# Kernel optimization log

Hardware: AMD Instinct MI355X
Metric: run time of the kernel (lower is better)

The kernel has to match this reference:

```python
import jax, jax.numpy as jnp
import numpy as np

B = 8192
T = 1000
STATE_DIM = 3
HIDDEN = 256
DT = 0.01


def setup_inputs() -> dict:
    key = jax.random.key(0)
    ks = jax.random.split(key, 7)
    initial_state = jax.random.normal(ks[0], (B, STATE_DIM), dtype=jnp.float32)
    t_grid = (jnp.arange(T, dtype=jnp.float32) * DT)
    s = 0.1  # small init scale keeps the ODE well-behaved over the grid
    W1 = jax.random.normal(ks[1], (STATE_DIM, HIDDEN), dtype=jnp.float32) * s
    b1 = jnp.zeros((HIDDEN,), dtype=jnp.float32)
    W2 = jax.random.normal(ks[2], (HIDDEN, HIDDEN), dtype=jnp.float32) * s
    b2 = jnp.zeros((HIDDEN,), dtype=jnp.float32)
    W3 = jax.random.normal(ks[3], (HIDDEN, STATE_DIM), dtype=jnp.float32) * s
    b3 = jnp.zeros((STATE_DIM,), dtype=jnp.float32)
    return {"initial_state": initial_state, "t_grid": t_grid,
            "W1": W1, "b1": b1, "W2": W2, "b2": b2, "W3": W3, "b3": b3}


def reference(initial_state, t_grid, W1, b1, W2, b2, W3, b3):
    # VectorFieldNet: state -> tanh MLP -> dstate/dt (autonomous; ignores t)
    def vf(s):  # s: [B, D]
        h = jnp.tanh(s @ W1 + b1)
        h = jnp.tanh(h @ W2 + b2)
        return h @ W3 + b3

    dts = t_grid[1:] - t_grid[:-1]  # [T-1]

    def step(cur, dt):
        k1 = vf(cur)
        k2 = vf(cur + 0.5 * dt * k1)
        k3 = vf(cur + 0.5 * dt * k2)
        k4 = vf(cur + dt * k3)
        nxt = cur + (dt / 6.0) * (k1 + 2.0 * k2 + 2.0 * k3 + k4)
        return nxt, nxt

    _, traj = jax.lax.scan(step, initial_state, dts)  # [T-1, B, D]
    rollout = jnp.concatenate([initial_state[None], traj], axis=0)  # [T, B, D]
    return jnp.transpose(rollout, (1, 0, 2))  # [B, T, D]
```

## Files before the change

kernel.cpp:

```cpp
#include <hip/hip_runtime.h>

typedef __attribute__((ext_vector_type(8))) short bf16x8;
typedef __attribute__((ext_vector_type(4))) float f32x4;
typedef __attribute__((ext_vector_type(2))) unsigned int uint2v;

union FU { unsigned int u[4]; uint4 q; bf16x8 v; };

__device__ inline unsigned int cvt_pk(float lo, float hi) {
    unsigned int r;
    asm("v_cvt_pk_bf16_f32 %0, %1, %2" : "=v"(r) : "v"(lo), "v"(hi));
    return r;
}

#define TWO_LOG2E 2.8853900817779268f
__device__ inline float tanh_fast(float x) {
#if __has_builtin(__builtin_amdgcn_exp2f)
    float e = __builtin_amdgcn_exp2f(x * TWO_LOG2E);
#else
    float e = __expf(x + x);
#endif
    return fmaf(-2.f, __builtin_amdgcn_rcpf(e + 1.f), 1.f);
}

__device__ inline float xor32_add(float p) {
    float c = p;
    asm("v_permlane32_swap_b32 %0, %1" : "+v"(c), "+v"(p));
    return p + c;
}

__device__ inline float xor16_add(float p) {
#if __has_builtin(__builtin_amdgcn_permlane16_swap)
    uint2v r = __builtin_amdgcn_permlane16_swap(__float_as_uint(p),
                                                __float_as_uint(p),
                                                false, false);
    return __uint_as_float(r[0]) + __uint_as_float(r[1]);
#else
    return p + __shfl_xor(p, 16);
#endif
}

__device__ inline void lds_barrier() {
    asm volatile("s_waitcnt lgkmcnt(0)\n\ts_barrier" ::: "memory");
}

#define TS 1000
#define ROWU 33
#define P2ROW 208

__global__ __launch_bounds__(512, 4)
void node_ode_kernel(const float* __restrict__ Ig, const float* __restrict__ tg,
                     const float* __restrict__ W1g, const float* __restrict__ b1g,
                     const float* __restrict__ W2g, const float* __restrict__ b2g,
                     const float* __restrict__ W3g, const float* __restrict__ b3g,
                     float* __restrict__ outp)
{
    __shared__ __align__(16) uint4 h1q[16 * ROWU];
    __shared__ __align__(16) char part2[16 * P2ROW];
    __shared__ float dtss[TS - 1];

    const int tid  = threadIdx.x;
    const int lane = tid & 63;
    const int wv   = tid >> 6;
    const int nb   = lane & 15;
    const int g4   = lane >> 4;
    const int bb0  = blockIdx.x * 16;

    const int wbase = nb * ROWU + wv * 4 + g4;
    const int rbase = nb * ROWU + g4;
    char* const prow = part2 + nb * P2ROW;

    for (int i = tid; i < TS - 1; i += 512) dtss[i] = tg[i + 1] - tg[i];

    const float b30 = b3g[0], b31 = b3g[1], b32 = b3g[2];

    float4 b2r0 = *(const float4*)&b2g[wv * 32 + g4 * 4];
    float4 b2r1 = *(const float4*)&b2g[wv * 32 + 16 + g4 * 4];

    float y00 = Ig[(bb0 + nb) * 3 + 0];
    float y01 = Ig[(bb0 + nb) * 3 + 1];
    float y02 = Ig[(bb0 + nb) * 3 + 2];
    if (tid < 16) {
        size_t o = (size_t)(bb0 + tid) * (TS * 3);
        outp[o + 0] = y00; outp[o + 1] = y01; outp[o + 2] = y02;
    }

    bf16x8 w2f[2][8];
    {
        const int ncb = wv * 32 + nb;
        #pragma unroll
        for (int mt = 0; mt < 2; ++mt) {
            #pragma unroll
            for (int ks = 0; ks < 8; ++ks) {
                FU f;
                #pragma unroll
                for (int jj = 0; jj < 4; ++jj) {
                    int k0 = ks * 32 + g4 * 8 + jj * 2;
                    f.u[jj] = cvt_pk(W2g[(size_t)k0 * 256 + ncb + mt * 16],
                                     W2g[(size_t)(k0 + 1) * 256 + ncb + mt * 16]);
                }
                w2f[mt][ks] = f.v;
            }
        }
    }

    bf16x8 w1a[2];
    {
        const int colb = wv * 32 + ((nb >> 2) << 3) + (nb & 3);
        #pragma unroll
        for (int mt = 0; mt < 2; ++mt) {
            const int col = colb + mt * 4;
            float w0 = W1g[col], w1 = W1g[256 + col], w2 = W1g[512 + col];
            float bb = b1g[col];
            FU f;
            if (g4 == 0) {
                f.u[0] = cvt_pk(w0, w1);
                f.u[1] = cvt_pk(w2, w0);
                f.u[2] = cvt_pk(w1, w2);
                f.u[3] = cvt_pk(bb, 0.f);
            } else if (g4 == 1) {
                unsigned int p01 = cvt_pk(w0, w1);
                unsigned int p2x = cvt_pk(w2, 0.f);
                float w0l = w0 - __uint_as_float(p01 << 16);
                float w1l = w1 - __uint_as_float(p01 & 0xFFFF0000u);
                float w2l = w2 - __uint_as_float(p2x << 16);
                f.u[0] = cvt_pk(w0l, w1l);
                f.u[1] = cvt_pk(w2l, 0.f);
                f.u[2] = 0u; f.u[3] = 0u;
            } else {
                f.u[0] = f.u[1] = f.u[2] = f.u[3] = 0u;
            }
            w1a[mt] = f.v;
        }
    }

    bf16x8 w3a;
    {
        FU f; f.u[0] = f.u[1] = f.u[2] = f.u[3] = 0u;
        if (nb < 6) {
            const int d = (nb < 3) ? nb : nb - 3;
            float w[8];
            #pragma unroll
            for (int j = 0; j < 8; ++j) {
                int ch = (j < 4) ? (wv * 32 + 4 * g4 + j)
                                 : (wv * 32 + 16 + 4 * g4 + (j - 4));
                w[j] = W3g[ch * 3 + d];
            }
            #pragma unroll
            for (int p = 0; p < 4; ++p) {
                unsigned int hp = cvt_pk(w[2 * p], w[2 * p + 1]);
                if (nb < 3) {
                    f.u[p] = hp;
                } else {
                    float l0 = w[2 * p]     - __uint_as_float(hp << 16);
                    float l1 = w[2 * p + 1] - __uint_as_float(hp & 0xFFFF0000u);
                    f.u[p] = cvt_pk(l0, l1);
                }
            }
        }
        w3a = f.v;
    }
    __syncthreads();

    auto EVAL = [&](float ycx, float ycy, float ycz,
                    float& kkx, float& kky, float& kkz) {
        {
            unsigned int u01  = cvt_pk(ycx, ycy);
            float yl0 = ycx - __uint_as_float(u01 << 16);
            float yl1 = ycy - __uint_as_float(u01 & 0xFFFF0000u);
            unsigned int u2l0 = cvt_pk(ycz, yl0);
            float yl2 = ycz - __uint_as_float(u2l0 << 16);
            unsigned int ull  = cvt_pk(yl1, yl2);
            FU bf;
            if (g4 == 0) {
                bf.u[0] = u01; bf.u[1] = u2l0; bf.u[2] = ull; bf.u[3] = 0x00003f80u;
            } else if (g4 == 1) {
                bf.u[0] = u01; bf.u[1] = u2l0 & 0x0000FFFFu; bf.u[2] = 0u; bf.u[3] = 0u;
            } else {
                bf.u[0] = bf.u[1] = bf.u[2] = bf.u[3] = 0u;
            }
            f32x4 dA = {0.f, 0.f, 0.f, 0.f};
            f32x4 dB = {0.f, 0.f, 0.f, 0.f};
            dA = __builtin_amdgcn_mfma_f32_16x16x32_bf16(w1a[0], bf.v, dA, 0, 0, 0);
            dB = __builtin_amdgcn_mfma_f32_16x16x32_bf16(w1a[1], bf.v, dB, 0, 0, 0);
            uint4 wq;
            wq.x = cvt_pk(tanh_fast(dA[0]), tanh_fast(dA[1]));
            wq.y = cvt_pk(tanh_fast(dA[2]), tanh_fast(dA[3]));
            wq.z = cvt_pk(tanh_fast(dB[0]), tanh_fast(dB[1]));
            wq.w = cvt_pk(tanh_fast(dB[2]), tanh_fast(dB[3]));
            h1q[wbase] = wq;
        }
        lds_barrier();

        {
            f32x4 acc0 = {b2r0.x, b2r0.y, b2r0.z, b2r0.w};
            f32x4 acc1 = {b2r1.x, b2r1.y, b2r1.z, b2r1.w};
            #pragma unroll
            for (int ks = 0; ks < 8; ++ks) {
                FU tm; tm.q = h1q[rbase + ks * 4];
                acc0 = __builtin_amdgcn_mfma_f32_16x16x32_bf16(w2f[0][ks], tm.v, acc0, 0, 0, 0);
                acc1 = __builtin_amdgcn_mfma_f32_16x16x32_bf16(w2f[1][ks], tm.v, acc1, 0, 0, 0);
            }
            FU pb;
            pb.u[0] = cvt_pk(tanh_fast(acc0[0]), tanh_fast(acc0[1]));
            pb.u[1] = cvt_pk(tanh_fast(acc0[2]), tanh_fast(acc0[3]));
            pb.u[2] = cvt_pk(tanh_fast(acc1[0]), tanh_fast(acc1[1]));
            pb.u[3] = cvt_pk(tanh_fast(acc1[2]), tanh_fast(acc1[3]));
            f32x4 pd = {0.f, 0.f, 0.f, 0.f};
            pd = __builtin_amdgcn_mfma_f32_16x16x32_bf16(w3a, pb.v, pd, 0, 0, 0);
            if (g4 == 0)
                *(float4*)(prow + wv * 16) = make_float4(pd[0], pd[1], pd[2], pd[3]);
            else if (g4 == 1)
                *(float2*)(prow + 128 + wv * 8) = make_float2(pd[0], pd[1]);
        }
        lds_barrier();

        {
            float4 q1 = *(const float4*)(prow + g4 * 16);
            float4 q2 = *(const float4*)(prow + 64 + g4 * 16);
            float4 q3 = *(const float4*)(prow + 128 + g4 * 16);
            float k0 = (q1.x + q2.x) + (q1.w + q2.w);
            float k1 = (q1.y + q2.y) + (q3.x + q3.z);
            float k2 = (q1.z + q2.z) + (q3.y + q3.w);
            k0 = xor16_add(k0); k1 = xor16_add(k1); k2 = xor16_add(k2);
            kkx = xor32_add(k0) + b30;
            kky = xor32_add(k1) + b31;
            kkz = xor32_add(k2) + b32;
        }
    };

    for (int t = 0; t < TS - 1; ++t) {
        const float dtc = dtss[t];
        const float hh = 0.5f * dtc;
        float k1x, k1y, k1z, k2x, k2y, k2z, k3x, k3y, k3z, k4x, k4y, k4z;
        EVAL(y00, y01, y02, k1x, k1y, k1z);
        EVAL(fmaf(hh, k1x, y00), fmaf(hh, k1y, y01), fmaf(hh, k1z, y02),
             k2x, k2y, k2z);
        EVAL(fmaf(hh, k2x, y00), fmaf(hh, k2y, y01), fmaf(hh, k2z, y02),
             k3x, k3y, k3z);
        EVAL(fmaf(dtc, k3x, y00), fmaf(dtc, k3y, y01), fmaf(dtc, k3z, y02),
             k4x, k4y, k4z);
        const float s = dtc * (1.f / 6.f);
        y00 = fmaf(s, (k1x + k4x) + 2.f * (k2x + k3x), y00);
        y01 = fmaf(s, (k1y + k4y) + 2.f * (k2y + k3y), y01);
        y02 = fmaf(s, (k1z + k4z) + 2.f * (k2z + k3z), y02);
        if ((wv == (t & 7)) && lane < 16) {
            size_t o = (size_t)(bb0 + nb) * (TS * 3) + (size_t)(t + 1) * 3;
            outp[o + 0] = y00; outp[o + 1] = y01; outp[o + 2] = y02;
        }
    }
}

extern "C" void kernel_launch(void* const* d_in, const int* in_sizes, int n_in,
                              void* d_out, int out_size, void* d_ws, size_t ws_size,
                              hipStream_t stream) {
    (void)in_sizes; (void)n_in; (void)d_ws; (void)ws_size; (void)out_size;
    const float* Ig  = (const float*)d_in[0];
    const float* tg  = (const float*)d_in[1];
    const float* W1g = (const float*)d_in[2];
    const float* b1g = (const float*)d_in[3];
    const float* W2g = (const float*)d_in[4];
    const float* b2g = (const float*)d_in[5];
    const float* W3g = (const float*)d_in[6];
    const float* b3g = (const float*)d_in[7];
    float* outp = (float*)d_out;

    dim3 grid(512), block(512);
    hipLaunchKernelGGL(node_ode_kernel, grid, block, 0, stream,
                       Ig, tg, W1g, b1g, W2g, b2g, W3g, b3g, outp);
}
```

Baseline: 7.271 ms.

## Interleave two batch tiles per block to overlap RK4 stage pipelines

Each block now handles 32 rows as two independent 16-row tiles, and the two tiles' MLP evaluations are software-pipelined across double-buffered LDS. The aim is to hide the serial dependency and barrier latency of each RK stage by running one tile's layer-2/3 work while the other tile's layer-1 and reduction proceed, cutting barriers per evaluation from three to two. The grid is halved to 256 blocks and launch bounds drop to 2 blocks per CU. That lowers the number of concurrent independent blocks and may raise register pressure.

```diff
diff --git a/kernel.cpp b/kernel.cpp
--- a/kernel.cpp
+++ b/kernel.cpp
@@ -44,18 +44,19 @@
 }
 
 #define TS 1000
+#define NEV ((TS - 1) * 4)
 #define ROWU 33
 #define P2ROW 208
 
-__global__ __launch_bounds__(512, 4)
+__global__ __launch_bounds__(512, 2)
 void node_ode_kernel(const float* __restrict__ Ig, const float* __restrict__ tg,
                      const float* __restrict__ W1g, const float* __restrict__ b1g,
                      const float* __restrict__ W2g, const float* __restrict__ b2g,
                      const float* __restrict__ W3g, const float* __restrict__ b3g,
                      float* __restrict__ outp)
 {
-    __shared__ __align__(16) uint4 h1q[16 * ROWU];
-    __shared__ __align__(16) char part2[16 * P2ROW];
+    __shared__ __align__(16) uint4 h1q[2][16 * ROWU];
+    __shared__ __align__(16) char part2[2][16 * P2ROW];
     __shared__ float dtss[TS - 1];
 
     const int tid  = threadIdx.x;
@@ -63,25 +64,35 @@
     const int wv   = tid >> 6;
     const int nb   = lane & 15;
     const int g4   = lane >> 4;
-    const int bb0  = blockIdx.x * 16;
-
-    const int wbase = nb * ROWU + wv * 4 + g4;
-    const int rbase = nb * ROWU + g4;
-    char* const prow = part2 + nb * P2ROW;
+    const int bb0  = blockIdx.x * 32;
+
+    const int wslot = nb * ROWU + wv * 4 + g4;
+    const int rslot = nb * ROWU + g4;
+    char* const prow0 = part2[0] + nb * P2ROW;
+    char* const prow1 = part2[1] + nb * P2ROW;
 
     for (int i = tid; i < TS - 1; i += 512) dtss[i] = tg[i + 1] - tg[i];
 
     const float b30 = b3g[0], b31 = b3g[1], b32 = b3g[2];
-
     float4 b2r0 = *(const float4*)&b2g[wv * 32 + g4 * 4];
     float4 b2r1 = *(const float4*)&b2g[wv * 32 + 16 + g4 * 4];
 
-    float y00 = Ig[(bb0 + nb) * 3 + 0];
-    float y01 = Ig[(bb0 + nb) * 3 + 1];
-    float y02 = Ig[(bb0 + nb) * 3 + 2];
-    if (tid < 16) {
+    float y0_0 = Ig[(bb0 + nb) * 3 + 0];
+    float y0_1 = Ig[(bb0 + nb) * 3 + 1];
+    float y0_2 = Ig[(bb0 + nb) * 3 + 2];
+    float y1_0 = Ig[(bb0 + 16 + nb) * 3 + 0];
+    float y1_1 = Ig[(bb0 + 16 + nb) * 3 + 1];
+    float y1_2 = Ig[(bb0 + 16 + nb) * 3 + 2];
+    float yc0_0 = y0_0, yc0_1 = y0_1, yc0_2 = y0_2;
+    float yc1_0 = y1_0, yc1_1 = y1_1, yc1_2 = y1_2;
+    float ks0_0 = 0.f, ks0_1 = 0.f, ks0_2 = 0.f;
+    float ks1_0 = 0.f, ks1_1 = 0.f, ks1_2 = 0.f;
+    if (tid < 32) {
         size_t o = (size_t)(bb0 + tid) * (TS * 3);
-        outp[o + 0] = y00; outp[o + 1] = y01; outp[o + 2] = y02;
+        float a0 = Ig[(bb0 + tid) * 3 + 0];
+        float a1 = Ig[(bb0 + tid) * 3 + 1];
+        float a2 = Ig[(bb0 + tid) * 3 + 2];
+        outp[o + 0] = a0; outp[o + 1] = a1; outp[o + 2] = a2;
     }
 
     bf16x8 w2f[2][8];
@@ -161,92 +172,126 @@
     }
     __syncthreads();
 
-    auto EVAL = [&](float ycx, float ycy, float ycz,
-                    float& kkx, float& kky, float& kkz) {
+    auto stageA = [&](float ycx, float ycy, float ycz, uint4* hb) {
+        unsigned int u01  = cvt_pk(ycx, ycy);
+        float yl0 = ycx - __uint_as_float(u01 << 16);
+        float yl1 = ycy - __uint_as_float(u01 & 0xFFFF0000u);
+        unsigned int u2l0 = cvt_pk(ycz, yl0);
+        float yl2 = ycz - __uint_as_float(u2l0 << 16);
+        unsigned int ull  = cvt_pk(yl1, yl2);
+        FU bf;
+        if (g4 == 0) {
+            bf.u[0] = u01; bf.u[1] = u2l0; bf.u[2] = ull; bf.u[3] = 0x00003f80u;
+        } else if (g4 == 1) {
+            bf.u[0] = u01; bf.u[1] = u2l0 & 0x0000FFFFu; bf.u[2] = 0u; bf.u[3] = 0u;
+        } else {
+            bf.u[0] = bf.u[1] = bf.u[2] = bf.u[3] = 0u;
+        }
+        f32x4 dA = {0.f, 0.f, 0.f, 0.f};
+        f32x4 dB = {0.f, 0.f, 0.f, 0.f};
+        dA = __builtin_amdgcn_mfma_f32_16x16x32_bf16(w1a[0], bf.v, dA, 0, 0, 0);
+        dB = __builtin_amdgcn_mfma_f32_16x16x32_bf16(w1a[1], bf.v, dB, 0, 0, 0);
+        uint4 wq;
+        wq.x = cvt_pk(tanh_fast(dA[0]), tanh_fast(dA[1]));
+        wq.y = cvt_pk(tanh_fast(dA[2]), tanh_fast(dA[3]));
+        wq.z = cvt_pk(tanh_fast(dB[0]), tanh_fast(dB[1]));
+        wq.w = cvt_pk(tanh_fast(dB[2]), tanh_fast(dB[3]));
+        hb[wslot] = wq;
+    };
+
+    auto stageB = [&](const uint4* hb, char* pw) {
+        f32x4 acc0 = {b2r0.x, b2r0.y, b2r0.z, b2r0.w};
+        f32x4 acc1 = {b2r1.x, b2r1.y, b2r1.z, b2r1.w};
+        #pragma unroll
+        for (int ks = 0; ks < 8; ++ks) {
+            FU tm; tm.q = hb[rslot + ks * 4];
+            acc0 = __builtin_amdgcn_mfma_f32_16x16x32_bf16(w2f[0][ks], tm.v, acc0, 0, 0, 0);
+            acc1 = __builtin_amdgcn_mfma_f32_16x16x32_bf16(w2f[1][ks], tm.v, acc1, 0, 0, 0);
+        }
+        FU pb;
+        pb.u[0] = cvt_pk(tanh_fast(acc0[0]), tanh_fast(acc0[1]));
+        pb.u[1] = cvt_pk(tanh_fast(acc0[2]), tanh_fast(acc0[3]));
+        pb.u[2] = cvt_pk(tanh_fast(acc1[0]), tanh_fast(acc1[1]));
+        pb.u[3] = cvt_pk(tanh_fast(acc1[2]), tanh_fast(acc1[3]));
+        f32x4 pd = {0.f, 0.f, 0.f, 0.f};
+        pd = __builtin_amdgcn_mfma_f32_16x16x32_bf16(w3a, pb.v, pd, 0, 0, 0);
+        if (g4 == 0)
+            *(float4*)(pw + wv * 16) = make_float4(pd[0], pd[1], pd[2], pd[3]);
+        else if (g4 == 1)
+            *(float2*)(pw + 128 + wv * 8) = make_float2(pd[0], pd[1]);
+    };
+
+    auto combine = [&](const char* pr, float& kkx, float& kky, float& kkz) {
+        float4 q1 = *(const float4*)(pr + g4 * 16);
+        float4 q2 = *(const float4*)(pr + 64 + g4 * 16);
+        float4 q3 = *(const float4*)(pr + 128 + g4 * 16);
+        float k0 = (q1.x + q2.x) + (q1.w + q2.w);
+        float k1 = (q1.y + q2.y) + (q3.x + q3.z);
+        float k2 = (q1.z + q2.z) + (q3.y + q3.w);
+        k0 = xor16_add(k0); k1 = xor16_add(k1); k2 = xor16_add(k2);
+        kkx = xor32_add(k0) + b30;
+        kky = xor32_add(k1) + b31;
+        kkz = xor32_add(k2) + b32;
+    };
+
+    auto advance = [&](int ev, float k0, float k1, float k2,
+                       float& y0, float& y1, float& y2,
+                       float& ks0, float& ks1, float& ks2,
+                       float& yc0, float& yc1, float& yc2, int rowoff) {
+        const int pph = ev & 3;
+        const int t = ev >> 2;
+        float dtc = dtss[t];
+        if (pph == 0) {
+            ks0 = k0; ks1 = k1; ks2 = k2;
+            float h = 0.5f * dtc;
+            yc0 = fmaf(h, k0, y0); yc1 = fmaf(h, k1, y1); yc2 = fmaf(h, k2, y2);
+        } else if (pph == 1) {
+            ks0 += 2.f * k0; ks1 += 2.f * k1; ks2 += 2.f * k2;
+            float h = 0.5f * dtc;
+            yc0 = fmaf(h, k0, y0); yc1 = fmaf(h, k1, y1); yc2 = fmaf(h, k2, y2);
+        } else if (pph == 2) {
+            ks0 += 2.f * k0; ks1 += 2.f * k1; ks2 += 2.f * k2;
+            yc0 = fmaf(dtc, k0, y0); yc1 = fmaf(dtc, k1, y1); yc2 = fmaf(dtc, k2, y2);
+        } else {
+            float s = dtc * (1.f / 6.f);
+            y0 = fmaf(s, ks0 + k0, y0);
+            y1 = fmaf(s, ks1 + k1, y1);
+            y2 = fmaf(s, ks2 + k2, y2);
+            yc0 = y0; yc1 = y1; yc2 = y2;
+            if ((wv == (t & 7)) && lane < 16) {
+                size_t o = (size_t)(bb0 + rowoff + nb) * (TS * 3) + (size_t)(t + 1) * 3;
+                outp[o + 0] = y0; outp[o + 1] = y1; outp[o + 2] = y2;
+            }
+        }
+    };
+
+    stageA(yc0_0, yc0_1, yc0_2, h1q[0]);
+    lds_barrier();
+    for (int ev = 0; ev < NEV; ++ev) {
+        stageB(h1q[0], prow0);
+        if (ev > 0) {
+            float k0, k1, k2;
+            combine(prow1, k0, k1, k2);
+            advance(ev - 1, k0, k1, k2, y1_0, y1_1, y1_2,
+                    ks1_0, ks1_1, ks1_2, yc1_0, yc1_1, yc1_2, 16);
+        }
+        stageA(yc1_0, yc1_1, yc1_2, h1q[1]);
+        lds_barrier();
+        stageB(h1q[1], prow1);
         {
-            unsigned int u01  = cvt_pk(ycx, ycy);
-            float yl0 = ycx - __uint_as_float(u01 << 16);
-            float yl1 = ycy - __uint_as_float(u01 & 0xFFFF0000u);
-            unsigned int u2l0 = cvt_pk(ycz, yl0);
-            float yl2 = ycz - __uint_as_float(u2l0 << 16);
-            unsigned int ull  = cvt_pk(yl1, yl2);
-            FU bf;
-            if (g4 == 0) {
-                bf.u[0] = u01; bf.u[1] = u2l0; bf.u[2] = ull; bf.u[3] = 0x00003f80u;
-            } else if (g4 == 1) {
-                bf.u[0] = u01; bf.u[1] = u2l0 & 0x0000FFFFu; bf.u[2] = 0u; bf.u[3] = 0u;
-            } else {
-                bf.u[0] = bf.u[1] = bf.u[2] = bf.u[3] = 0u;
-            }
-            f32x4 dA = {0.f, 0.f, 0.f, 0.f};
-            f32x4 dB = {0.f, 0.f, 0.f, 0.f};
-            dA = __builtin_amdgcn_mfma_f32_16x16x32_bf16(w1a[0], bf.v, dA, 0, 0, 0);
-            dB = __builtin_amdgcn_mfma_f32_16x16x32_bf16(w1a[1], bf.v, dB, 0, 0, 0);
-            uint4 wq;
-            wq.x = cvt_pk(tanh_fast(dA[0]), tanh_fast(dA[1]));
-            wq.y = cvt_pk(tanh_fast(dA[2]), tanh_fast(dA[3]));
-            wq.z = cvt_pk(tanh_fast(dB[0]), tanh_fast(dB[1]));
-            wq.w = cvt_pk(tanh_fast(dB[2]), tanh_fast(dB[3]));
-            h1q[wbase] = wq;
-        }
+            float k0, k1, k2;
+            combine(prow0, k0, k1, k2);
+            advance(ev, k0, k1, k2, y0_0, y0_1, y0_2,
+                    ks0_0, ks0_1, ks0_2, yc0_0, yc0_1, yc0_2, 0);
+        }
+        if (ev < NEV - 1) stageA(yc0_0, yc0_1, yc0_2, h1q[0]);
         lds_barrier();
-
-        {
-            f32x4 acc0 = {b2r0.x, b2r0.y, b2r0.z, b2r0.w};
-            f32x4 acc1 = {b2r1.x, b2r1.y, b2r1.z, b2r1.w};
-            #pragma unroll
-            for (int ks = 0; ks < 8; ++ks) {
-                FU tm; tm.q = h1q[rbase + ks * 4];
-                acc0 = __builtin_amdgcn_mfma_f32_16x16x32_bf16(w2f[0][ks], tm.v, acc0, 0, 0, 0);
-                acc1 = __builtin_amdgcn_mfma_f32_16x16x32_bf16(w2f[1][ks], tm.v, acc1, 0, 0, 0);
-            }
-            FU pb;
-            pb.u[0] = cvt_pk(tanh_fast(acc0[0]), tanh_fast(acc0[1]));
-            pb.u[1] = cvt_pk(tanh_fast(acc0[2]), tanh_fast(acc0[3]));
-            pb.u[2] = cvt_pk(tanh_fast(acc1[0]), tanh_fast(acc1[1]));
-            pb.u[3] = cvt_pk(tanh_fast(acc1[2]), tanh_fast(acc1[3]));
-            f32x4 pd = {0.f, 0.f, 0.f, 0.f};
-            pd = __builtin_amdgcn_mfma_f32_16x16x32_bf16(w3a, pb.v, pd, 0, 0, 0);
-            if (g4 == 0)
-                *(float4*)(prow + wv * 16) = make_float4(pd[0], pd[1], pd[2], pd[3]);
-            else if (g4 == 1)
-                *(float2*)(prow + 128 + wv * 8) = make_float2(pd[0], pd[1]);
-        }
-        lds_barrier();
-
-        {
-            float4 q1 = *(const float4*)(prow + g4 * 16);
-            float4 q2 = *(const float4*)(prow + 64 + g4 * 16);
-            float4 q3 = *(const float4*)(prow + 128 + g4 * 16);
-            float k0 = (q1.x + q2.x) + (q1.w + q2.w);
-            float k1 = (q1.y + q2.y) + (q3.x + q3.z);
-            float k2 = (q1.z + q2.z) + (q3.y + q3.w);
-            k0 = xor16_add(k0); k1 = xor16_add(k1); k2 = xor16_add(k2);
-            kkx = xor32_add(k0) + b30;
-            kky = xor32_add(k1) + b31;
-            kkz = xor32_add(k2) + b32;
-        }
-    };
-
-    for (int t = 0; t < TS - 1; ++t) {
-        const float dtc = dtss[t];
-        const float hh = 0.5f * dtc;
-        float k1x, k1y, k1z, k2x, k2y, k2z, k3x, k3y, k3z, k4x, k4y, k4z;
-        EVAL(y00, y01, y02, k1x, k1y, k1z);
-        EVAL(fmaf(hh, k1x, y00), fmaf(hh, k1y, y01), fmaf(hh, k1z, y02),
-             k2x, k2y, k2z);
-        EVAL(fmaf(hh, k2x, y00), fmaf(hh, k2y, y01), fmaf(hh, k2z, y02),
-             k3x, k3y, k3z);
-        EVAL(fmaf(dtc, k3x, y00), fmaf(dtc, k3y, y01), fmaf(dtc, k3z, y02),
-             k4x, k4y, k4z);
-        const float s = dtc * (1.f / 6.f);
-        y00 = fmaf(s, (k1x + k4x) + 2.f * (k2x + k3x), y00);
-        y01 = fmaf(s, (k1y + k4y) + 2.f * (k2y + k3y), y01);
-        y02 = fmaf(s, (k1z + k4z) + 2.f * (k2z + k3z), y02);
-        if ((wv == (t & 7)) && lane < 16) {
-            size_t o = (size_t)(bb0 + nb) * (TS * 3) + (size_t)(t + 1) * 3;
-            outp[o + 0] = y00; outp[o + 1] = y01; outp[o + 2] = y02;
-        }
+    }
+    {
+        float k0, k1, k2;
+        combine(prow1, k0, k1, k2);
+        advance(NEV - 1, k0, k1, k2, y1_0, y1_1, y1_2,
+                ks1_0, ks1_1, ks1_2, yc1_0, yc1_1, yc1_2, 16);
     }
 }
 
@@ -264,7 +309,7 @@
     const float* b3g = (const float*)d_in[7];
     float* outp = (float*)d_out;
 
-    dim3 grid(512), block(512);
+    dim3 grid(256), block(512);
     hipLaunchKernelGGL(node_ode_kernel, grid, block, 0, stream,
                        Ig, tg, W1g, b1g, W2g, b2g, W3g, b3g, outp);
 }
```

New measurement: 8.944 ms. 1.23x slower.
